# Optimization experiments

Hardware: AMD Instinct MI355X
Metric: run time of the kernel (lower is better)

Reference implementation:

```python
import jax, jax.numpy as jnp
import numpy as np

B, T, F, H = 2048, 256, 128, 64


def setup_inputs() -> dict:
    key = jax.random.key(0)
    ks = jax.random.split(key, 7)
    s_ih = 1.0 / np.sqrt(H)
    return {
        "x": jax.random.normal(ks[0], (B, T, F), dtype=jnp.float32),
        "w_ih": jax.random.uniform(ks[1], (3 * H, F), jnp.float32, -s_ih, s_ih),
        "w_hh": jax.random.uniform(ks[2], (3 * H, H), jnp.float32, -s_ih, s_ih),
        "b_ih": jax.random.uniform(ks[3], (3 * H,), jnp.float32, -s_ih, s_ih),
        "b_hh": jax.random.uniform(ks[4], (3 * H,), jnp.float32, -s_ih, s_ih),
        "fc_w": jax.random.uniform(ks[5], (1, H), jnp.float32, -s_ih, s_ih),
        "fc_b": jax.random.uniform(ks[6], (1,), jnp.float32, -s_ih, s_ih),
    }


def _gru_last_hidden(x, w_ih, w_hh, b_ih, b_hh):
    # Precompute input projections for all timesteps: [B,T,3H] -> scan over T
    gx = jnp.einsum("btf,gf->btg", x, w_ih) + b_ih  # g = 3H
    gx = jnp.transpose(gx, (1, 0, 2))  # [T, B, 3H]
    h0 = jnp.zeros((x.shape[0], w_hh.shape[1]), dtype=x.dtype)
    Hd = w_hh.shape[1]

    def step(h, gx_t):
        gh = h @ w_hh.T + b_hh  # [B, 3H]
        rx, zx, nx = gx_t[:, :Hd], gx_t[:, Hd:2 * Hd], gx_t[:, 2 * Hd:]
        rh, zh, nh = gh[:, :Hd], gh[:, Hd:2 * Hd], gh[:, 2 * Hd:]
        r = jax.nn.sigmoid(rx + rh)
        z = jax.nn.sigmoid(zx + zh)
        n = jnp.tanh(nx + r * nh)
        h_new = (1.0 - z) * n + z * h
        return h_new, None

    h_last, _ = jax.lax.scan(step, h0, gx)
    return h_last  # [B, H]


def reference(x, w_ih, w_hh, b_ih, b_hh, fc_w, fc_b):
    # eval mode: dropout is identity
    h_last = _gru_last_hidden(x, w_ih, w_hh, b_ih, b_hh)
    return h_last @ fc_w.T + fc_b  # [B, 1]
```

## Files before the change

### kernel.cpp

```cpp
#include <hip/hip_runtime.h>

#define B_ 2048
#define T_ 256
#define F_ 128
#define H_ 64

typedef __attribute__((ext_vector_type(8))) short short8;
typedef __attribute__((ext_vector_type(4))) float f32x4;

__device__ __forceinline__ unsigned int rne2(float fa, float fb) {
    unsigned int ua = __float_as_uint(fa);
    unsigned int ub = __float_as_uint(fb);
    ua = ua + 0x7fffu + ((ua >> 16) & 1u);
    ub = ub + 0x7fffu + ((ub >> 16) & 1u);
    return (ua >> 16) | (ub & 0xffff0000u);
}
__device__ __forceinline__ float sigmoid_f(float v) {
    return __fdividef(1.0f, 1.0f + __expf(-v));
}
__device__ __forceinline__ float tanh_f(float v) {
    return 1.0f - __fdividef(2.0f, 1.0f + __expf(2.0f * v));
}

__global__ __launch_bounds__(256, 2) void gru_fused(
    const float* __restrict__ x, const float* __restrict__ w_ih,
    const float* __restrict__ w_hh, const float* __restrict__ b_ih,
    const float* __restrict__ b_hh, const float* __restrict__ fc_w,
    const float* __restrict__ fc_b, float* __restrict__ out)
{
    __shared__ __align__(16) short wihf[12 * 4 * 64 * 8];
    __shared__ __align__(16) short hhi_l[2][4][72];
    __shared__ __align__(16) short hlo_l[2][4][72];
    __shared__ float wred[4][4];

    const int tid = threadIdx.x;
    const int wv  = tid >> 6;
    const int j   = tid & 63;
    const int q   = j >> 4;
    const int c   = j & 15;
    const int brow = blockIdx.x * 4;

    for (int s = tid; s < 12 * 4 * 64; s += 256) {
        const int n = s >> 8, ks = (s >> 6) & 3, L = s & 63;
        const float* wp = w_ih + (n * 16 + (L & 15)) * F_ + ks * 32 + ((L >> 4) * 8);
        const float4 a = *(const float4*)wp;
        const float4 b = *(const float4*)(wp + 4);
        union { short8 v; unsigned int u[4]; } fr;
        fr.u[0] = rne2(a.x, a.y); fr.u[1] = rne2(a.z, a.w);
        fr.u[2] = rne2(b.x, b.y); fr.u[3] = rne2(b.z, b.w);
        *(short8*)&wihf[s * 8] = fr.v;
    }
    for (int i = tid; i < 2 * 4 * 72; i += 256) {
        ((short*)hhi_l)[i] = 0;
        ((short*)hlo_l)[i] = 0;
    }

    const int d0 = wv * 16 + c;
    const float bxr = b_ih[d0],       bgr = b_hh[d0];
    const float bxz = b_ih[64 + d0],  bgz = b_hh[64 + d0];
    const float bxn = b_ih[128 + d0], bgn = b_hh[128 + d0];
    const float fw0 = fc_w[d0];

    short8 wh[3][2];
    #pragma unroll
    for (int g = 0; g < 3; ++g) {
        #pragma unroll
        for (int ks2 = 0; ks2 < 2; ++ks2) {
            const float* wp = w_hh + (g * 64 + wv * 16 + c) * H_ + ks2 * 32 + q * 8;
            const float4 a = *(const float4*)wp;
            const float4 b = *(const float4*)(wp + 4);
            union { short8 v; unsigned int u[4]; } fr;
            fr.u[0] = rne2(a.x, a.y); fr.u[1] = rne2(a.z, a.w);
            fr.u[2] = rne2(b.x, b.y); fr.u[3] = rne2(b.z, b.w);
            wh[g][ks2] = fr.v;
        }
    }

    const int xrow = (j & 15) & 3;
    const int xsl  = (j & 15) >> 3;
    const float* xlane = x + ((size_t)(brow + xrow) * T_ + xsl) * F_ + q * 8;

    __syncthreads();

    float4 XA[8], XB[8];
    {
        const float* lp = xlane;
        #pragma unroll
        for (int ks = 0; ks < 4; ++ks) {
            XA[2 * ks]     = *(const float4*)(lp + ks * 32);
            XA[2 * ks + 1] = *(const float4*)(lp + ks * 32 + 4);
        }
        lp = xlane + 2 * F_;
        #pragma unroll
        for (int ks = 0; ks < 4; ++ks) {
            XB[2 * ks]     = *(const float4*)(lp + ks * 32);
            XB[2 * ks + 1] = *(const float4*)(lp + ks * 32 + 4);
        }
    }

    short8 af[4], hh[2], hl[2];
    const short8 z8 = {0, 0, 0, 0, 0, 0, 0, 0};
    hh[0] = z8; hh[1] = z8; hl[0] = z8; hl[1] = z8;

    auto cvtbuf = [&](float4 (&Xv)[8]) {
        #pragma unroll
        for (int ks = 0; ks < 4; ++ks) {
            union { short8 v; unsigned int u[4]; } fr;
            fr.u[0] = rne2(Xv[2 * ks].x,     Xv[2 * ks].y);
            fr.u[1] = rne2(Xv[2 * ks].z,     Xv[2 * ks].w);
            fr.u[2] = rne2(Xv[2 * ks + 1].x, Xv[2 * ks + 1].y);
            fr.u[3] = rne2(Xv[2 * ks + 1].z, Xv[2 * ks + 1].w);
            af[ks] = fr.v;
        }
    };
    cvtbuf(XA);

    auto do_macro = [&](float4 (&Xre)[8], float4 (&Xcv)[8], int t0) {
        f32x4 axr = {bxr, bxr, bxr, bxr};
        f32x4 axz = {bxz, bxz, bxz, bxz};
        f32x4 axn = {bxn, bxn, bxn, bxn};
        {
            const int tr = (0 + wv) * 2048;
            const int tz = (4 + wv) * 2048;
            const int tn = (8 + wv) * 2048;
            #pragma unroll
            for (int ks = 0; ks < 4; ++ks) {
                axr = __builtin_amdgcn_mfma_f32_16x16x32_bf16(
                    af[ks], *(const short8*)&wihf[tr + ks * 512 + j * 8], axr, 0, 0, 0);
                axz = __builtin_amdgcn_mfma_f32_16x16x32_bf16(
                    af[ks], *(const short8*)&wihf[tz + ks * 512 + j * 8], axz, 0, 0, 0);
                axn = __builtin_amdgcn_mfma_f32_16x16x32_bf16(
                    af[ks], *(const short8*)&wihf[tn + ks * 512 + j * 8], axn, 0, 0, 0);
            }
        }
        {
            int tl = t0 + 4; if (tl > 254) tl = 254;
            const float* lp = xlane + (size_t)tl * F_;
            #pragma unroll
            for (int ks = 0; ks < 4; ++ks) {
                Xre[2 * ks]     = *(const float4*)(lp + ks * 32);
                Xre[2 * ks + 1] = *(const float4*)(lp + ks * 32 + 4);
            }
        }
        auto step = [&](int s) {
            f32x4 agr = {bgr, bgr, bgr, bgr};
            f32x4 agz = {bgz, bgz, bgz, bgz};
            f32x4 agn = {bgn, bgn, bgn, bgn};
            #pragma unroll
            for (int ks2 = 0; ks2 < 2; ++ks2) {
                agr = __builtin_amdgcn_mfma_f32_16x16x32_bf16(hh[ks2], wh[0][ks2], agr, 0, 0, 0);
                agr = __builtin_amdgcn_mfma_f32_16x16x32_bf16(hl[ks2], wh[0][ks2], agr, 0, 0, 0);
                agz = __builtin_amdgcn_mfma_f32_16x16x32_bf16(hh[ks2], wh[1][ks2], agz, 0, 0, 0);
                agz = __builtin_amdgcn_mfma_f32_16x16x32_bf16(hl[ks2], wh[1][ks2], agz, 0, 0, 0);
                agn = __builtin_amdgcn_mfma_f32_16x16x32_bf16(hh[ks2], wh[2][ks2], agn, 0, 0, 0);
                agn = __builtin_amdgcn_mfma_f32_16x16x32_bf16(hl[ks2], wh[2][ks2], agn, 0, 0, 0);
            }
            if ((q >> 1) == s) {
                const int rowsel = q & 1;
                #pragma unroll
                for (int rl = 0; rl < 2; ++rl) {
                    const int row = rowsel * 2 + rl;
                    const int e   = rowsel * 2 + rl;
                    const float vr  = axr[e] + agr[e];
                    const float vz  = axz[e] + agz[e];
                    const float r = sigmoid_f(vr);
                    const float z = sigmoid_f(vz);
                    const float n = tanh_f(axn[e] + r * agn[e]);
                    const float hp =
                        __uint_as_float(((unsigned int)(unsigned short)hhi_l[s][row][d0]) << 16) +
                        __uint_as_float(((unsigned int)(unsigned short)hlo_l[s][row][d0]) << 16);
                    const float hn = n + z * (hp - n);
                    const unsigned int uh = __float_as_uint(hn);
                    const unsigned int rr = uh + 0x7fffu + ((uh >> 16) & 1u);
                    const float hif = __uint_as_float(rr & 0xffff0000u);
                    const float lof = hn - hif;
                    const unsigned int ul = __float_as_uint(lof);
                    const unsigned int r2 = ul + 0x7fffu + ((ul >> 16) & 1u);
                    hhi_l[s ^ 1][row][d0] = (short)(rr >> 16);
                    hlo_l[s ^ 1][row][d0] = (short)(r2 >> 16);
                }
            }
            __syncthreads();
            #pragma unroll
            for (int ks2 = 0; ks2 < 2; ++ks2) {
                hh[ks2] = *(const short8*)&hhi_l[s ^ 1][xrow][ks2 * 32 + q * 8];
                hl[ks2] = *(const short8*)&hlo_l[s ^ 1][xrow][ks2 * 32 + q * 8];
            }
        };
        step(0);
        step(1);
        cvtbuf(Xcv);
    };

    #pragma unroll 1
    for (int t0 = 0; t0 < T_; t0 += 4) {
        do_macro(XA, XB, t0);
        do_macro(XB, XA, t0 + 2);
    }

    {
        const int row = q;
        const float hv0 =
            __uint_as_float(((unsigned int)(unsigned short)hhi_l[0][row][d0]) << 16) +
            __uint_as_float(((unsigned int)(unsigned short)hlo_l[0][row][d0]) << 16);
        float partial = hv0 * fw0;
        #pragma unroll
        for (int m = 1; m <= 8; m <<= 1) partial += __shfl_xor(partial, m, 64);
        if (c == 0) wred[wv][q] = partial;
        __syncthreads();
        if (tid < 4)
            out[brow + tid] = wred[0][tid] + wred[1][tid] + wred[2][tid] + wred[3][tid] + fc_b[0];
    }
}

extern "C" void kernel_launch(void* const* d_in, const int* in_sizes, int n_in,
                              void* d_out, int out_size, void* d_ws, size_t ws_size,
                              hipStream_t stream)
{
    (void)in_sizes; (void)n_in; (void)out_size; (void)d_ws; (void)ws_size;
    const float* x    = (const float*)d_in[0];
    const float* w_ih = (const float*)d_in[1];
    const float* w_hh = (const float*)d_in[2];
    const float* b_ih = (const float*)d_in[3];
    const float* b_hh = (const float*)d_in[4];
    const float* fc_w = (const float*)d_in[5];
    const float* fc_b = (const float*)d_in[6];
    float* out = (float*)d_out;

    gru_fused<<<dim3(B_ / 4), 256, 0, stream>>>(
        x, w_ih, w_hh, b_ih, b_hh, fc_w, fc_b, out);
}
```

Measured before the change: 582.2 us.

## Assign one batch row per wavefront with full-width recurrent MFMA per step

Each wavefront now owns one batch row and computes all 192 gate outputs itself, packing the bf16 hi/lo parts of h as separate MFMA rows so one pass covers both. The input projection for eight timesteps is computed in a single burst of MFMAs with merged biases, and the x loads are spread across the steps. This removes cross-wave exchange of h, but each wave now issues 24 MFMAs per step while most of the output rows are wasted. It also keeps many more weight registers live, which risks spills and lower occupancy. A block-wide __syncthreads still runs every step even though the waves no longer share data.

```diff
diff --git a/kernel.cpp b/kernel.cpp
--- a/kernel.cpp
+++ b/kernel.cpp
@@ -20,6 +20,9 @@
 }
 __device__ __forceinline__ float tanh_f(float v) {
     return 1.0f - __fdividef(2.0f, 1.0f + __expf(2.0f * v));
+}
+__device__ __forceinline__ float b2f(short v) {
+    return __uint_as_float(((unsigned int)(unsigned short)v) << 16);
 }
 
 __global__ __launch_bounds__(256, 2) void gru_fused(
@@ -29,16 +32,15 @@
     const float* __restrict__ fc_b, float* __restrict__ out)
 {
     __shared__ __align__(16) short wihf[12 * 4 * 64 * 8];
-    __shared__ __align__(16) short hhi_l[2][4][72];
-    __shared__ __align__(16) short hlo_l[2][4][72];
-    __shared__ float wred[4][4];
+    __shared__ __align__(16) short ha[4][16][72];
+    __shared__ float bias_l[12][16];
 
     const int tid = threadIdx.x;
     const int wv  = tid >> 6;
-    const int j   = tid & 63;
-    const int q   = j >> 4;
-    const int c   = j & 15;
-    const int brow = blockIdx.x * 4;
+    const int l   = tid & 63;
+    const int c   = l & 15;
+    const int lq  = l >> 4;
+    const int row = blockIdx.x * 4 + wv;
 
     for (int s = tid; s < 12 * 4 * 64; s += 256) {
         const int n = s >> 8, ks = (s >> 6) & 3, L = s & 63;
@@ -50,166 +52,142 @@
         fr.u[2] = rne2(b.x, b.y); fr.u[3] = rne2(b.z, b.w);
         *(short8*)&wihf[s * 8] = fr.v;
     }
-    for (int i = tid; i < 2 * 4 * 72; i += 256) {
-        ((short*)hhi_l)[i] = 0;
-        ((short*)hlo_l)[i] = 0;
-    }
-
-    const int d0 = wv * 16 + c;
-    const float bxr = b_ih[d0],       bgr = b_hh[d0];
-    const float bxz = b_ih[64 + d0],  bgz = b_hh[64 + d0];
-    const float bxn = b_ih[128 + d0], bgn = b_hh[128 + d0];
-    const float fw0 = fc_w[d0];
-
-    short8 wh[3][2];
+    for (int i = tid; i < 4 * 16 * 72; i += 256) ((short*)ha)[i] = 0;
+    if (tid < 192) {
+        const int t = tid >> 4, cc = tid & 15;
+        const int d = t * 16 + cc;
+        bias_l[t][cc] = b_ih[d] + (t < 8 ? b_hh[d] : 0.0f);
+    }
+
+    float bnh[4];
     #pragma unroll
-    for (int g = 0; g < 3; ++g) {
-        #pragma unroll
-        for (int ks2 = 0; ks2 < 2; ++ks2) {
-            const float* wp = w_hh + (g * 64 + wv * 16 + c) * H_ + ks2 * 32 + q * 8;
+    for (int i = 0; i < 4; ++i) bnh[i] = b_hh[128 + i * 16 + c];
+
+    short8 whf[12][2];
+    #pragma unroll
+    for (int t = 0; t < 12; ++t) {
+        #pragma unroll
+        for (int k2 = 0; k2 < 2; ++k2) {
+            const float* wp = w_hh + (t * 16 + c) * H_ + k2 * 32 + lq * 8;
             const float4 a = *(const float4*)wp;
             const float4 b = *(const float4*)(wp + 4);
             union { short8 v; unsigned int u[4]; } fr;
             fr.u[0] = rne2(a.x, a.y); fr.u[1] = rne2(a.z, a.w);
             fr.u[2] = rne2(b.x, b.y); fr.u[3] = rne2(b.z, b.w);
-            wh[g][ks2] = fr.v;
-        }
-    }
-
-    const int xrow = (j & 15) & 3;
-    const int xsl  = (j & 15) >> 3;
-    const float* xlane = x + ((size_t)(brow + xrow) * T_ + xsl) * F_ + q * 8;
+            whf[t][k2] = fr.v;
+        }
+    }
+
+    const int tau_c = (c & 3) | ((c >> 3) << 2);
+    const float* xlane = x + ((size_t)row * T_ + tau_c) * F_ + lq * 8;
+    short* hap = &ha[wv][0][0];
+    const int ha_rd = (c & 11) * 72 + lq * 8;
 
     __syncthreads();
 
-    float4 XA[8], XB[8];
+    float4 Xh[4];
+    short8 af[4];
+    auto loadx = [&](const float* lp, int ksb) {
+        #pragma unroll
+        for (int k2 = 0; k2 < 2; ++k2) {
+            Xh[2 * k2]     = *(const float4*)(lp + (ksb + k2) * 32);
+            Xh[2 * k2 + 1] = *(const float4*)(lp + (ksb + k2) * 32 + 4);
+        }
+    };
+    auto cvt2 = [&](int ksb) {
+        #pragma unroll
+        for (int k2 = 0; k2 < 2; ++k2) {
+            union { short8 v; unsigned int u[4]; } fr;
+            fr.u[0] = rne2(Xh[2 * k2].x,     Xh[2 * k2].y);
+            fr.u[1] = rne2(Xh[2 * k2].z,     Xh[2 * k2].w);
+            fr.u[2] = rne2(Xh[2 * k2 + 1].x, Xh[2 * k2 + 1].y);
+            fr.u[3] = rne2(Xh[2 * k2 + 1].z, Xh[2 * k2 + 1].w);
+            af[ksb + k2] = fr.v;
+        }
+    };
+    loadx(xlane, 0); cvt2(0); loadx(xlane, 2); cvt2(2);
+
+    f32x4 GXA[12];
+    const f32x4 zc = {0.f, 0.f, 0.f, 0.f};
+    auto burst = [&]() {
+        #pragma unroll
+        for (int t = 0; t < 12; ++t) {
+            const float bv = bias_l[t][c];
+            GXA[t] = (f32x4){bv, bv, bv, bv};
+        }
+        #pragma unroll
+        for (int ks = 0; ks < 4; ++ks) {
+            #pragma unroll
+            for (int t = 0; t < 12; ++t)
+                GXA[t] = __builtin_amdgcn_mfma_f32_16x16x32_bf16(
+                    af[ks], *(const short8*)&wihf[(t * 4 + ks) * 512 + l * 8], GXA[t], 0, 0, 0);
+        }
+    };
+    burst();
+
+    #pragma unroll 1
+    for (int m = 0; m < 32; ++m) {
+        #pragma unroll
+        for (int t2 = 0; t2 < 2; ++t2) {
+            #pragma unroll
+            for (int si = 0; si < 4; ++si) {
+                const int tau = t2 * 4 + si;
+                const int g2  = ((tau + 1) & 7) >> 2;
+                const short8 hA0 = *(const short8*)&hap[ha_rd];
+                const short8 hA1 = *(const short8*)&hap[ha_rd + 32];
+                float hp[4];
+                #pragma unroll
+                for (int i = 0; i < 4; ++i)
+                    hp[i] = b2f(hap[(8 * t2) * 72 + i * 16 + c]) +
+                            b2f(hap[(8 * t2 + 1) * 72 + i * 16 + c]);
+                f32x4 GH[12];
+                #pragma unroll
+                for (int t = 0; t < 12; ++t)
+                    GH[t] = __builtin_amdgcn_mfma_f32_16x16x32_bf16(hA0, whf[t][0], zc, 0, 0, 0);
+                #pragma unroll
+                for (int t = 0; t < 12; ++t)
+                    GH[t] = __builtin_amdgcn_mfma_f32_16x16x32_bf16(hA1, whf[t][1], GH[t], 0, 0, 0);
+                if (tau == 1 && m < 31)
+                    loadx(xlane + (size_t)(8 * (m + 1)) * F_, 0);
+                if (tau == 3 && m < 31) {
+                    cvt2(0);
+                    loadx(xlane + (size_t)(8 * (m + 1)) * F_, 2);
+                }
+                if (tau == 5 && m < 31)
+                    cvt2(2);
+                if (lq == 2 * t2) {
+                    #pragma unroll
+                    for (int i = 0; i < 4; ++i) {
+                        const float ghr = GH[i][0]     + GH[i][1];
+                        const float ghz = GH[4 + i][0] + GH[4 + i][1];
+                        const float ghn = GH[8 + i][0] + GH[8 + i][1];
+                        const float r = sigmoid_f(GXA[i][si] + ghr);
+                        const float z = sigmoid_f(GXA[4 + i][si] + ghz);
+                        const float n = tanh_f(GXA[8 + i][si] + r * (ghn + bnh[i]));
+                        const float hn = n + z * (hp[i] - n);
+                        const unsigned int uh = __float_as_uint(hn);
+                        const unsigned int rr = uh + 0x7fffu + ((uh >> 16) & 1u);
+                        const float hif = __uint_as_float(rr & 0xffff0000u);
+                        const float lof = hn - hif;
+                        const unsigned int ul = __float_as_uint(lof);
+                        const unsigned int r2 = ul + 0x7fffu + ((ul >> 16) & 1u);
+                        hap[(8 * g2)     * 72 + i * 16 + c] = (short)(rr >> 16);
+                        hap[(8 * g2 + 1) * 72 + i * 16 + c] = (short)(r2 >> 16);
+                    }
+                }
+                asm volatile("" ::: "memory");
+                __syncthreads();
+            }
+        }
+        if (m < 31) burst();
+    }
+
     {
-        const float* lp = xlane;
-        #pragma unroll
-        for (int ks = 0; ks < 4; ++ks) {
-            XA[2 * ks]     = *(const float4*)(lp + ks * 32);
-            XA[2 * ks + 1] = *(const float4*)(lp + ks * 32 + 4);
-        }
-        lp = xlane + 2 * F_;
-        #pragma unroll
-        for (int ks = 0; ks < 4; ++ks) {
-            XB[2 * ks]     = *(const float4*)(lp + ks * 32);
-            XB[2 * ks + 1] = *(const float4*)(lp + ks * 32 + 4);
-        }
-    }
-
-    short8 af[4], hh[2], hl[2];
-    const short8 z8 = {0, 0, 0, 0, 0, 0, 0, 0};
-    hh[0] = z8; hh[1] = z8; hl[0] = z8; hl[1] = z8;
-
-    auto cvtbuf = [&](float4 (&Xv)[8]) {
-        #pragma unroll
-        for (int ks = 0; ks < 4; ++ks) {
-            union { short8 v; unsigned int u[4]; } fr;
-            fr.u[0] = rne2(Xv[2 * ks].x,     Xv[2 * ks].y);
-            fr.u[1] = rne2(Xv[2 * ks].z,     Xv[2 * ks].w);
-            fr.u[2] = rne2(Xv[2 * ks + 1].x, Xv[2 * ks + 1].y);
-            fr.u[3] = rne2(Xv[2 * ks + 1].z, Xv[2 * ks + 1].w);
-            af[ks] = fr.v;
-        }
-    };
-    cvtbuf(XA);
-
-    auto do_macro = [&](float4 (&Xre)[8], float4 (&Xcv)[8], int t0) {
-        f32x4 axr = {bxr, bxr, bxr, bxr};
-        f32x4 axz = {bxz, bxz, bxz, bxz};
-        f32x4 axn = {bxn, bxn, bxn, bxn};
-        {
-            const int tr = (0 + wv) * 2048;
-            const int tz = (4 + wv) * 2048;
-            const int tn = (8 + wv) * 2048;
-            #pragma unroll
-            for (int ks = 0; ks < 4; ++ks) {
-                axr = __builtin_amdgcn_mfma_f32_16x16x32_bf16(
-                    af[ks], *(const short8*)&wihf[tr + ks * 512 + j * 8], axr, 0, 0, 0);
-                axz = __builtin_amdgcn_mfma_f32_16x16x32_bf16(
-                    af[ks], *(const short8*)&wihf[tz + ks * 512 + j * 8], axz, 0, 0, 0);
-                axn = __builtin_amdgcn_mfma_f32_16x16x32_bf16(
-                    af[ks], *(const short8*)&wihf[tn + ks * 512 + j * 8], axn, 0, 0, 0);
-            }
-        }
-        {
-            int tl = t0 + 4; if (tl > 254) tl = 254;
-            const float* lp = xlane + (size_t)tl * F_;
-            #pragma unroll
-            for (int ks = 0; ks < 4; ++ks) {
-                Xre[2 * ks]     = *(const float4*)(lp + ks * 32);
-                Xre[2 * ks + 1] = *(const float4*)(lp + ks * 32 + 4);
-            }
-        }
-        auto step = [&](int s) {
-            f32x4 agr = {bgr, bgr, bgr, bgr};
-            f32x4 agz = {bgz, bgz, bgz, bgz};
-            f32x4 agn = {bgn, bgn, bgn, bgn};
-            #pragma unroll
-            for (int ks2 = 0; ks2 < 2; ++ks2) {
-                agr = __builtin_amdgcn_mfma_f32_16x16x32_bf16(hh[ks2], wh[0][ks2], agr, 0, 0, 0);
-                agr = __builtin_amdgcn_mfma_f32_16x16x32_bf16(hl[ks2], wh[0][ks2], agr, 0, 0, 0);
-                agz = __builtin_amdgcn_mfma_f32_16x16x32_bf16(hh[ks2], wh[1][ks2], agz, 0, 0, 0);
-                agz = __builtin_amdgcn_mfma_f32_16x16x32_bf16(hl[ks2], wh[1][ks2], agz, 0, 0, 0);
-                agn = __builtin_amdgcn_mfma_f32_16x16x32_bf16(hh[ks2], wh[2][ks2], agn, 0, 0, 0);
-                agn = __builtin_amdgcn_mfma_f32_16x16x32_bf16(hl[ks2], wh[2][ks2], agn, 0, 0, 0);
-            }
-            if ((q >> 1) == s) {
-                const int rowsel = q & 1;
-                #pragma unroll
-                for (int rl = 0; rl < 2; ++rl) {
-                    const int row = rowsel * 2 + rl;
-                    const int e   = rowsel * 2 + rl;
-                    const float vr  = axr[e] + agr[e];
-                    const float vz  = axz[e] + agz[e];
-                    const float r = sigmoid_f(vr);
-                    const float z = sigmoid_f(vz);
-                    const float n = tanh_f(axn[e] + r * agn[e]);
-                    const float hp =
-                        __uint_as_float(((unsigned int)(unsigned short)hhi_l[s][row][d0]) << 16) +
-                        __uint_as_float(((unsigned int)(unsigned short)hlo_l[s][row][d0]) << 16);
-                    const float hn = n + z * (hp - n);
-                    const unsigned int uh = __float_as_uint(hn);
-                    const unsigned int rr = uh + 0x7fffu + ((uh >> 16) & 1u);
-                    const float hif = __uint_as_float(rr & 0xffff0000u);
-                    const float lof = hn - hif;
-                    const unsigned int ul = __float_as_uint(lof);
-                    const unsigned int r2 = ul + 0x7fffu + ((ul >> 16) & 1u);
-                    hhi_l[s ^ 1][row][d0] = (short)(rr >> 16);
-                    hlo_l[s ^ 1][row][d0] = (short)(r2 >> 16);
-                }
-            }
-            __syncthreads();
-            #pragma unroll
-            for (int ks2 = 0; ks2 < 2; ++ks2) {
-                hh[ks2] = *(const short8*)&hhi_l[s ^ 1][xrow][ks2 * 32 + q * 8];
-                hl[ks2] = *(const short8*)&hlo_l[s ^ 1][xrow][ks2 * 32 + q * 8];
-            }
-        };
-        step(0);
-        step(1);
-        cvtbuf(Xcv);
-    };
-
-    #pragma unroll 1
-    for (int t0 = 0; t0 < T_; t0 += 4) {
-        do_macro(XA, XB, t0);
-        do_macro(XB, XA, t0 + 2);
-    }
-
-    {
-        const int row = q;
-        const float hv0 =
-            __uint_as_float(((unsigned int)(unsigned short)hhi_l[0][row][d0]) << 16) +
-            __uint_as_float(((unsigned int)(unsigned short)hlo_l[0][row][d0]) << 16);
-        float partial = hv0 * fw0;
-        #pragma unroll
-        for (int m = 1; m <= 8; m <<= 1) partial += __shfl_xor(partial, m, 64);
-        if (c == 0) wred[wv][q] = partial;
-        __syncthreads();
-        if (tid < 4)
-            out[brow + tid] = wred[0][tid] + wred[1][tid] + wred[2][tid] + wred[3][tid] + fc_b[0];
+        const float hv = b2f(hap[l]) + b2f(hap[72 + l]);
+        float partial = hv * fc_w[l];
+        #pragma unroll
+        for (int msk = 1; msk <= 32; msk <<= 1) partial += __shfl_xor(partial, msk, 64);
+        if (l == 0) out[row] = partial + fc_b[0];
     }
 }
 
```

After: 801.4 us. 37.7% more time.
